# Kernel tuning notes

Measured on AMD Instinct MI355X. Metric: run time of the kernel, lower is better.

The kernel has to match this reference:

```python
import jax, jax.numpy as jnp
import numpy as np

B, C, D = 512, 50000, 256
N_LOADED = 40000


def setup_inputs() -> dict:
    key = jax.random.key(0)
    k1, k2, k3, k4 = jax.random.split(key, 4)
    visual_feats = jax.random.normal(k1, (B, D), dtype=jnp.float32)
    text_feats = jax.random.normal(k2, (C, D), dtype=jnp.float32)
    # sparse multi-hot labels; force class 0 positive for every row so the
    # positive set (intersected with loaded ids) is never empty
    batch_label = (jax.random.uniform(k3, (B, C)) < 0.02).astype(jnp.int32)
    batch_label = batch_label.at[:, 0].set(1)
    # distinct loaded class ids; force id 0 to be loaded
    ids = jax.random.permutation(k4, C)[:N_LOADED].astype(jnp.int32)
    ids = jnp.sort(ids).at[0].set(0)
    return {
        "visual_feats": visual_feats,
        "text_feats": text_feats,
        "batch_label": batch_label,
        "class_ids_loaded": ids,
        "d_space": D,
    }


def reference(visual_feats, text_feats, batch_label, class_ids_loaded, d_space):
    num_classes = text_feats.shape[0]
    # membership mask for loaded class ids (the set() intersection in torch)
    loaded = jnp.zeros((num_classes,), dtype=bool).at[class_ids_loaded].set(True)

    # cosine similarity; note: torch adds 1e-6 eps only to text-feature norms
    v = visual_feats / jnp.linalg.norm(visual_feats, axis=1, keepdims=True)
    t = text_feats / (1e-6 + jnp.linalg.norm(text_feats, axis=1, keepdims=True))
    S = v @ t.T  # [B, C]

    pos = (batch_label != 0) & loaded[None, :]  # ragged positive sets, as mask
    neg = (batch_label == 0) & loaded[None, :]  # ragged negative sets, as mask

    # denominator: sum of exp(sim) over negatives, per row
    denom = jnp.sum(jnp.where(neg, jnp.exp(S), 0.0), axis=1)  # [B]
    n_pos = jnp.sum(pos, axis=1).astype(S.dtype)  # [B]

    # per-row loss: mean over positives of -log(exp(s_p)/denom) = log(denom)-s_p
    per_row = jnp.sum(jnp.where(pos, jnp.log(denom)[:, None] - S, 0.0), axis=1) / n_pos
    return jnp.mean(per_row).reshape(1)
```

## Files before the change

### kernel.cpp

```cpp
#include <hip/hip_runtime.h>
#include <math.h>

#define D_DIM 256
#define TM 128
#define TN 128
#define BK 32
#define NBP 392

typedef __attribute__((ext_vector_type(8))) short short8;
typedef __attribute__((ext_vector_type(4))) float floatx4;
typedef unsigned long long u64;

__device__ __forceinline__ unsigned short f2bf(float f) {
    unsigned int u = __float_as_uint(f);
    u += 0x7FFFu + ((u >> 16) & 1u);
    return (unsigned short)(u >> 16);
}

__device__ __forceinline__ void gload16(const void* g, void* lds) {
    __builtin_amdgcn_global_load_lds(
        (const __attribute__((address_space(1))) unsigned int*)g,
        (__attribute__((address_space(3))) unsigned int*)lds, 16, 0, 0);
}

__global__ __launch_bounds__(256) void prep_rows(
    const float* __restrict__ V, const float* __restrict__ T,
    const int* __restrict__ ids,
    u64* __restrict__ loadedmask, unsigned int* __restrict__ cntG,
    unsigned short* __restrict__ Vb, unsigned short* __restrict__ Tb,
    float* __restrict__ gaccum, unsigned int* __restrict__ gcount,
    int B, int C, int n_loaded, int WPR) {
    const int tid  = threadIdx.x;
    const int lane = tid & 63;
    int ptid = blockIdx.x * 256 + tid;
    if (ptid == 0) { *gcount = 0u; *gaccum = 0.f; }
    if (ptid < B) cntG[ptid] = 0u;
    if (ptid < WPR) {
        int base = ptid << 6;
        int lo = 0, hi = n_loaded;
        while (lo < hi) { int mid = (lo + hi) >> 1; if (ids[mid] < base) lo = mid + 1; else hi = mid; }
        u64 m = 0;
        for (int i = lo; i < n_loaded; ++i) {
            int v = ids[i]; if (v >= base + 64) break;
            m |= 1ull << (v - base);
        }
        loadedmask[ptid] = m;
    }
    int wave = ptid >> 6;
    if (wave >= B + C) return;
    bool isV = wave < B;
    const float* src = isV ? (V + (size_t)wave * D_DIM)
                           : (T + (size_t)(wave - B) * D_DIM);
    float4 x = ((const float4*)src)[lane];
    float ss = x.x * x.x + x.y * x.y + x.z * x.z + x.w * x.w;
    #pragma unroll
    for (int off = 32; off > 0; off >>= 1) ss += __shfl_xor(ss, off);
    float nrm = sqrtf(ss);
    float s = isV ? (1.0f / nrm) : (1.0f / (1e-6f + nrm));
    ushort4 o;
    o.x = f2bf(x.x * s); o.y = f2bf(x.y * s);
    o.z = f2bf(x.z * s); o.w = f2bf(x.w * s);
    unsigned short* dst = isV ? (Vb + (size_t)wave * D_DIM)
                              : (Tb + (size_t)(wave - B) * D_DIM);
    ((ushort4*)dst)[lane] = o;
}

__global__ __launch_bounds__(256) void gemm_fused(
    const unsigned short* __restrict__ Vb, const unsigned short* __restrict__ Tb,
    const int* __restrict__ label, const u64* __restrict__ loadedmask,
    float* __restrict__ denomP, float* __restrict__ posP,
    unsigned int* __restrict__ cntG, int C, int WPR) {
    __shared__ unsigned short As[2][TM * BK];
    __shared__ unsigned short Bs[2][TN * BK];
    __shared__ float sDen[TM], sPos[TM];
    __shared__ int sCnt[TM];

    const int tid  = threadIdx.x;
    const int lane = tid & 63;
    const int w    = tid >> 6;
    const int m0 = blockIdx.x * TM;
    const int n0 = blockIdx.y * TN;

    if (tid < TM) { sDen[tid] = 0.f; sPos[tid] = 0.f; sCnt[tid] = 0; }

    const int wm = (w >> 1) * 64;
    const int wn = (w & 1) * 64;
    const int fr = lane & 15;
    const int quad = lane >> 4;

    const u64 loadedw = loadedmask[(n0 + wn) >> 6];
    const int* lp = label + (size_t)(m0 + wm + lane) * C;
    const int nBase = n0 + wn;
    u64 praw = 0;
    #pragma unroll
    for (int k = 0; k < 16; ++k) {
        const int col0 = nBase + 4 * k;
        unsigned int nib = 0;
        if (col0 + 3 < C) {
            int4 v = *(const int4*)(lp + col0);
            nib = (v.x ? 1u : 0u) | (v.y ? 2u : 0u) | (v.z ? 4u : 0u) | (v.w ? 8u : 0u);
        } else {
            if (col0 + 0 < C && lp[col0 + 0]) nib |= 1u;
            if (col0 + 1 < C && lp[col0 + 1]) nib |= 2u;
            if (col0 + 2 < C && lp[col0 + 2]) nib |= 4u;
            if (col0 + 3 < C && lp[col0 + 3]) nib |= 8u;
        }
        praw |= (u64)nib << (4 * k);
    }

    const int sra = lane >> 2;
    const int kc  = (lane & 3) * 8;
    int ga  = m0 + w * 32 + sra;
    int gb0 = n0 + w * 32 + sra;
    int gb1 = gb0 + 16;
    if (gb0 >= C) gb0 = C - 1;
    if (gb1 >= C) gb1 = C - 1;
    const unsigned short* gA0 = Vb + (size_t)ga * D_DIM + kc;
    const unsigned short* gA1 = gA0 + (size_t)16 * D_DIM;
    const unsigned short* gB0 = Tb + (size_t)gb0 * D_DIM + kc;
    const unsigned short* gB1 = Tb + (size_t)gb1 * D_DIM + kc;
    const int lofsA = w * 32 * BK;
    const int lofsB = w * 32 * BK;

    floatx4 acc[4][4];
    #pragma unroll
    for (int mi = 0; mi < 4; mi++)
        #pragma unroll
        for (int ni = 0; ni < 4; ni++) acc[mi][ni] = (floatx4)0.f;

    gload16(gA0, &As[0][lofsA]);
    gload16(gA1, &As[0][lofsA + 16 * BK]);
    gload16(gB0, &Bs[0][lofsB]);
    gload16(gB1, &Bs[0][lofsB + 16 * BK]);
    __syncthreads();

    #pragma unroll
    for (int kt = 0; kt < D_DIM / BK; ++kt) {
        const int cur = kt & 1;
        if (kt < D_DIM / BK - 1) {
            const int kb = (kt + 1) * BK;
            gload16(gA0 + kb, &As[cur ^ 1][lofsA]);
            gload16(gA1 + kb, &As[cur ^ 1][lofsA + 16 * BK]);
            gload16(gB0 + kb, &Bs[cur ^ 1][lofsB]);
            gload16(gB1 + kb, &Bs[cur ^ 1][lofsB + 16 * BK]);
        }
        short8 af[4], bf[4];
        #pragma unroll
        for (int mi = 0; mi < 4; mi++)
            af[mi] = *(const short8*)&As[cur][(wm + mi * 16 + fr) * BK + quad * 8];
        #pragma unroll
        for (int ni = 0; ni < 4; ni++)
            bf[ni] = *(const short8*)&Bs[cur][(wn + ni * 16 + fr) * BK + quad * 8];
        #pragma unroll
        for (int mi = 0; mi < 4; mi++)
            #pragma unroll
            for (int ni = 0; ni < 4; ni++)
                acc[mi][ni] = __builtin_amdgcn_mfma_f32_16x16x32_bf16(
                    af[mi], bf[ni], acc[mi][ni], 0, 0, 0);
        __syncthreads();
    }

    atomicAdd(&sCnt[wm + lane], (int)__popcll(praw & loadedw));
    #pragma unroll
    for (int mi = 0; mi < 4; mi++) {
        #pragma unroll
        for (int i = 0; i < 4; i++) {
            const int rloc = mi * 16 + quad * 4 + i;
            const int mloc = wm + rloc;
            const u64 pr = __shfl(praw, rloc);
            const u64 posw = pr & loadedw;
            const u64 negw = loadedw & ~pr;
            float den = 0.f, pos = 0.f;
            #pragma unroll
            for (int ni = 0; ni < 4; ni++) {
                const float s = acc[mi][ni][i];
                const int bit = ni * 16 + fr;
                if ((negw >> bit) & 1) den += __expf(s);
                if ((posw >> bit) & 1) pos += s;
            }
            #pragma unroll
            for (int off = 8; off >= 1; off >>= 1) {
                den += __shfl_xor(den, off);
                pos += __shfl_xor(pos, off);
            }
            if (fr == 0) {
                if (den != 0.f) atomicAdd(&sDen[mloc], den);
                if (pos != 0.f) atomicAdd(&sPos[mloc], pos);
            }
        }
    }
    __syncthreads();
    if (tid < TM) {
        denomP[(size_t)(m0 + tid) * NBP + blockIdx.y] = sDen[tid];
        posP[(size_t)(m0 + tid) * NBP + blockIdx.y]   = sPos[tid];
        if (sCnt[tid]) atomicAdd(&cntG[m0 + tid], (unsigned int)sCnt[tid]);
    }
}

__global__ void reduce_rows(const float* __restrict__ denomP, const float* __restrict__ posP,
                            const unsigned int* __restrict__ cntG,
                            float* __restrict__ gaccum, unsigned int* __restrict__ gcount,
                            float* __restrict__ out, int B, int NB) {
    __shared__ float bsum[4];
    int wv   = threadIdx.x >> 6;
    int row  = blockIdx.x * 4 + wv;
    int lane = threadIdx.x & 63;
    float den = 0.f, pos = 0.f;
    if (row < B) {
        for (int bn = lane; bn < NB; bn += 64) {
            den += denomP[(size_t)row * NBP + bn];
            pos += posP[(size_t)row * NBP + bn];
        }
        #pragma unroll
        for (int off = 32; off > 0; off >>= 1) {
            den += __shfl_xor(den, off);
            pos += __shfl_xor(pos, off);
        }
    }
    if (lane == 0) bsum[wv] = (row < B) ? (logf(den) - pos / (float)cntG[row]) : 0.f;
    __syncthreads();
    if (threadIdx.x == 0) {
        float s = bsum[0] + bsum[1] + bsum[2] + bsum[3];
        atomicAdd(gaccum, s);
        __threadfence();
        unsigned int old = atomicAdd(gcount, 1u);
        if (old == gridDim.x - 1) {
            float tot = atomicAdd(gaccum, 0.0f);
            out[0] = tot / (float)B;
        }
    }
}

extern "C" void kernel_launch(void* const* d_in, const int* in_sizes, int n_in,
                              void* d_out, int out_size, void* d_ws, size_t ws_size,
                              hipStream_t stream) {
    const float* V     = (const float*)d_in[0];
    const float* T     = (const float*)d_in[1];
    const int*   label = (const int*)d_in[2];
    const int*   ids   = (const int*)d_in[3];
    int B = in_sizes[0] / D_DIM;
    int C = in_sizes[1] / D_DIM;
    int n_loaded = in_sizes[3];
    int WPR = (C + 63) >> 6;
    int NB  = (C + TN - 1) / TN;

    char* ws = (char*)d_ws;
    float*        gaccum = (float*)(ws + 0);
    unsigned int* gcount = (unsigned int*)(ws + 8);
    unsigned int* cntG   = (unsigned int*)(ws + 64);
    u64*   loadedmask = (u64*)(ws + 4096);
    unsigned short* Vb = (unsigned short*)(ws + 16384);
    unsigned short* Tb = (unsigned short*)(ws + 278528);
    float* denomP  = (float*)(ws + 25878528);
    float* posP    = (float*)(ws + 26681344);

    int prep_blocks = ((B + C) * 64 + 255) / 256;
    prep_rows<<<prep_blocks, 256, 0, stream>>>(
        V, T, ids, loadedmask, cntG, Vb, Tb, gaccum, gcount,
        B, C, n_loaded, WPR);

    dim3 grid(B / TM, NB);
    gemm_fused<<<grid, 256, 0, stream>>>(Vb, Tb, label, loadedmask,
                                         denomP, posP, cntG, C, WPR);

    reduce_rows<<<(B + 3) / 4, 256, 0, stream>>>(denomP, posP, cntG,
                                                 gaccum, gcount, (float*)d_out, B, NB);
}
```

Measured before the change: 273.3 us.

## Interleave label loads into GEMM loop and XOR-swizzle LDS tiles

Moves the per-tile label mask loads out of the prologue and spreads them over the first four k-iterations of the MFMA loop, packing them into bits one iteration later. This hides global label latency behind matrix work. It also XOR-swizzles the K-chunk placement in LDS on both the async-load and fragment-read sides to cut bank conflicts. The cost is higher register pressure from holding the int4 label buffers across iterations.

```diff
diff --git a/kernel.cpp b/kernel.cpp
--- a/kernel.cpp
+++ b/kernel.cpp
@@ -91,25 +91,9 @@
     const u64 loadedw = loadedmask[(n0 + wn) >> 6];
     const int* lp = label + (size_t)(m0 + wm + lane) * C;
     const int nBase = n0 + wn;
-    u64 praw = 0;
-    #pragma unroll
-    for (int k = 0; k < 16; ++k) {
-        const int col0 = nBase + 4 * k;
-        unsigned int nib = 0;
-        if (col0 + 3 < C) {
-            int4 v = *(const int4*)(lp + col0);
-            nib = (v.x ? 1u : 0u) | (v.y ? 2u : 0u) | (v.z ? 4u : 0u) | (v.w ? 8u : 0u);
-        } else {
-            if (col0 + 0 < C && lp[col0 + 0]) nib |= 1u;
-            if (col0 + 1 < C && lp[col0 + 1]) nib |= 2u;
-            if (col0 + 2 < C && lp[col0 + 2]) nib |= 4u;
-            if (col0 + 3 < C && lp[col0 + 3]) nib |= 8u;
-        }
-        praw |= (u64)nib << (4 * k);
-    }
 
     const int sra = lane >> 2;
-    const int kc  = (lane & 3) * 8;
+    const int kc  = (((lane & 3) ^ (sra & 3)) * 8);
     int ga  = m0 + w * 32 + sra;
     int gb0 = n0 + w * 32 + sra;
     int gb1 = gb0 + 16;
@@ -134,6 +118,9 @@
     gload16(gB1, &Bs[0][lofsB + 16 * BK]);
     __syncthreads();
 
+    u64 praw = 0;
+    int4 lv[4];
+
     #pragma unroll
     for (int kt = 0; kt < D_DIM / BK; ++kt) {
         const int cur = kt & 1;
@@ -144,13 +131,39 @@
             gload16(gB0 + kb, &Bs[cur ^ 1][lofsB]);
             gload16(gB1 + kb, &Bs[cur ^ 1][lofsB + 16 * BK]);
         }
+        if (kt >= 1 && kt <= 4) {
+            #pragma unroll
+            for (int j = 0; j < 4; ++j) {
+                const int kk = (kt - 1) * 4 + j;
+                unsigned int nib =
+                    (lv[j].x ? 1u : 0u) | (lv[j].y ? 2u : 0u) |
+                    (lv[j].z ? 4u : 0u) | (lv[j].w ? 8u : 0u);
+                praw |= (u64)nib << (4 * kk);
+            }
+        }
+        if (kt <= 3) {
+            #pragma unroll
+            for (int j = 0; j < 4; ++j) {
+                const int col0 = nBase + 4 * (kt * 4 + j);
+                if (col0 + 3 < C) {
+                    lv[j] = *(const int4*)(lp + col0);
+                } else {
+                    lv[j].x = (col0 + 0 < C) ? lp[col0 + 0] : 0;
+                    lv[j].y = (col0 + 1 < C) ? lp[col0 + 1] : 0;
+                    lv[j].z = (col0 + 2 < C) ? lp[col0 + 2] : 0;
+                    lv[j].w = (col0 + 3 < C) ? lp[col0 + 3] : 0;
+                }
+            }
+        }
         short8 af[4], bf[4];
         #pragma unroll
         for (int mi = 0; mi < 4; mi++)
-            af[mi] = *(const short8*)&As[cur][(wm + mi * 16 + fr) * BK + quad * 8];
+            af[mi] = *(const short8*)
+                &As[cur][(wm + mi * 16 + fr) * BK + (quad ^ (fr & 3)) * 8];
         #pragma unroll
         for (int ni = 0; ni < 4; ni++)
-            bf[ni] = *(const short8*)&Bs[cur][(wn + ni * 16 + fr) * BK + quad * 8];
+            bf[ni] = *(const short8*)
+                &Bs[cur][(wn + ni * 16 + fr) * BK + (quad ^ (fr & 3)) * 8];
         #pragma unroll
         for (int mi = 0; mi < 4; mi++)
             #pragma unroll
```

Measured after the change: 278.3 us. Within noise of the previous version (+1.8%).
